# Performance work log

Measured on AMD Instinct MI355X. Metric: run time of the kernel, lower is better.

The kernel has to match this reference:

```python
import jax, jax.numpy as jnp
import numpy as np

SHRINK_THRES = 0.0025
EPS = 1e-12


def setup_inputs() -> dict:
    key = jax.random.key(0)
    k1, k2 = jax.random.split(key)
    N, C, H, W = 32, 256, 32, 32
    M = 2000
    x = jax.random.normal(k1, (N, C, H, W), dtype=jnp.float32)
    # torch init: uniform(-stdv, stdv), stdv = 1/sqrt(fea_dim)
    stdv = 1.0 / np.sqrt(C)
    weight = jax.random.uniform(k2, (M, C), dtype=jnp.float32, minval=-stdv, maxval=stdv)
    return {"x": x, "weight": weight}


def hard_shrink_relu(a, lambd=SHRINK_THRES, epsilon=EPS):
    d = a - lambd
    return jax.nn.relu(d) * a / (jnp.abs(d) + epsilon)


def reference(x, weight):
    N, C, H, W = x.shape
    M = weight.shape[0]
    # N x C x H x W -> (N*H*W) x C
    xt = jnp.transpose(x, (0, 2, 3, 1)).reshape(-1, C)  # (T, C)
    att = xt @ weight.T                                  # (T, M)
    att = jax.nn.softmax(att, axis=1)
    att = hard_shrink_relu(att)
    # L1 normalize over memory dim (torch F.normalize p=1, eps=1e-12)
    att = att / jnp.maximum(jnp.sum(jnp.abs(att), axis=1, keepdims=True), 1e-12)
    y = att @ weight                                     # (T, C)
    y = y.reshape(N, H, W, C).transpose(0, 3, 1, 2)      # N x C x H x W
    att = att.reshape(N, H, W, M).transpose(0, 3, 1, 2)  # N x M x H x W
    return (y, att)
```

## Files before the change

kernel.cpp:

```cpp
#include <hip/hip_runtime.h>

typedef _Float16 f16x8 __attribute__((ext_vector_type(8)));
typedef float    f32x4 __attribute__((ext_vector_type(4)));

constexpr int Nn = 32, Cc = 256, HW = 1024, Mm = 2000, Tt = 32768;
constexpr int TB = 64;
constexpr int XROW = 264;
constexpr int YROW = 257;
constexpr int LCAP = 768;
constexpr int NT = 63;
constexpr float LAMBDA = 0.0025f;
constexpr float PLO = LAMBDA * (1.0f - 3e-3f);
constexpr float PHI = LAMBDA * (1.0f + 3e-3f);
constexpr float ECUT = 4.8f;
constexpr float SCL = 4096.0f, ISCL = 1.0f / 4096.0f;

__global__ void wcvt_kernel(const float* __restrict__ w,
                            _Float16* __restrict__ whi, _Float16* __restrict__ wlo) {
  int i = blockIdx.x * 256 + threadIdx.x;
  if (i < Mm * Cc) {
    float v = w[i];
    _Float16 h = (_Float16)v;
    whi[i] = h;
    wlo[i] = (_Float16)((v - (float)h) * SCL);
  }
}

__device__ __forceinline__ void gl_lds16(const void* g, void* l) {
  __builtin_amdgcn_global_load_lds(
      (const __attribute__((address_space(1))) void*)g,
      (__attribute__((address_space(3))) void*)l, 16, 0, 0);
}

__global__ __launch_bounds__(512, 4)
void fused_mem_kernel(const float* __restrict__ x, const float* __restrict__ wgt,
                      const _Float16* __restrict__ whi, const _Float16* __restrict__ wlo,
                      float* __restrict__ y_out, float* __restrict__ att_out) {
  __shared__ __align__(16) float bufB[TB * XROW];
  __shared__ int   lm[LCAP];
  __shared__ float le[LCAP];
  __shared__ float la[LCAP];
  __shared__ float Zred[128];
  __shared__ float invZ[TB];
  __shared__ float l1s[TB];
  __shared__ float dens[TB];
  __shared__ int   lcnt;
  _Float16* Xh = (_Float16*)bufB;
  _Float16* Xl = Xh + TB * XROW;
  float*    yL = bufB;
  char*     Bb = (char*)bufB;

  const int tid = threadIdx.x;
  const int wv  = tid >> 6;
  const int l   = tid & 63;
  const int qw  = l >> 4;
  const int lr  = l & 15;
  const int tg  = wv & 3;
  const int mh  = wv >> 2;
  const int t0  = blockIdx.x * TB;
  const int n   = t0 >> 10;
  const int hw0 = t0 & 1023;

  if (tid == 0) lcnt = 0;
  if (tid < TB) l1s[tid] = 0.f;

  {
    const int h = tid & 63, cb = tid >> 6;
    const float* xp = x + ((size_t)n * Cc) * HW + hw0 + h;
    #pragma unroll
    for (int j = 0; j < 32; ++j) {
      int c = cb * 32 + j;
      float v = xp[(size_t)c * HW];
      _Float16 hh = (_Float16)v;
      Xh[h * XROW + c] = hh;
      Xl[h * XROW + c] = (_Float16)((v - (float)hh) * SCL);
    }
  }
  __syncthreads();

  f16x8 ahi[8], alo[8];
  #pragma unroll
  for (int ks = 0; ks < 8; ++ks) {
    ahi[ks] = *(const f16x8*)&Xh[(tg * 16 + lr) * XROW + ks * 32 + qw * 8];
    alo[ks] = *(const f16x8*)&Xl[(tg * 16 + lr) * XROW + ks * 32 + qw * 8];
  }
  __syncthreads();

  auto stage = [&](int b, int tile) {
    char* base = Bb + b * 32768;
    #pragma unroll
    for (int i = 0; i < 4; ++i) {
      const int bu = i * 512 + wv * 64;
      const int u2 = (bu + l) & 1023;
      const int row = u2 >> 5, chunk = u2 & 31;
      int mrow = tile * 32 + row; mrow = mrow < Mm ? mrow : (Mm - 1);
      const char* src = (const char*)(i < 2 ? whi : wlo)
                      + (size_t)mrow * 512 + ((chunk ^ (row & 7)) << 4);
      gl_lds16(src, base + bu * 16);
    }
  };

  stage(0, 0);
  __syncthreads();

  float zp[4] = {0.f, 0.f, 0.f, 0.f};
  const int rrow = mh * 16 + lr;
  const int rsw  = rrow & 7;
  int cur = 0;
  for (int t = 0; t < NT; ++t) {
    if (t + 1 < NT) stage(cur ^ 1, t + 1);

    {
      int m = t * 32 + (tid >> 4);
      if (m < Mm) {
        f32x4 z4 = {0.f, 0.f, 0.f, 0.f};
        *(f32x4*)(att_out + ((size_t)(n * Mm + m)) * HW + hw0 + ((tid & 15) << 2)) = z4;
      }
    }

    if (mh == 0 || t < NT - 1) {
      const char* bb = Bb + cur * 32768;
      f16x8 bh[8], bl[8];
      #pragma unroll
      for (int ks = 0; ks < 8; ++ks) {
        const int ch = (((ks * 4 + qw) ^ rsw) << 4);
        bh[ks] = *(const f16x8*)(bb + rrow * 512 + ch);
        bl[ks] = *(const f16x8*)(bb + 16384 + rrow * 512 + ch);
      }
      f32x4 ahh = {0.f, 0.f, 0.f, 0.f};
      f32x4 axl = {0.f, 0.f, 0.f, 0.f};
      f32x4 alh = {0.f, 0.f, 0.f, 0.f};
      #pragma unroll
      for (int ks = 0; ks < 8; ++ks) {
        ahh = __builtin_amdgcn_mfma_f32_16x16x32_f16(ahi[ks], bh[ks], ahh, 0, 0, 0);
        axl = __builtin_amdgcn_mfma_f32_16x16x32_f16(ahi[ks], bl[ks], axl, 0, 0, 0);
        alh = __builtin_amdgcn_mfma_f32_16x16x32_f16(alo[ks], bh[ks], alh, 0, 0, 0);
      }
      const int mrow_ = t * 32 + rrow;
      #pragma unroll
      for (int r = 0; r < 4; ++r) {
        float s = fmaf(axl[r] + alh[r], ISCL, ahh[r]);
        float e = __expf(s);
        zp[r] += e;
        if (e > ECUT) {
          int slot = atomicAdd(&lcnt, 1);
          if (slot < LCAP) { lm[slot] = ((tg * 16 + qw * 4 + r) << 16) | mrow_; le[slot] = e; }
        }
      }
    }
    __syncthreads();
    cur ^= 1;
  }

  #pragma unroll
  for (int o = 1; o < 16; o <<= 1)
    #pragma unroll
    for (int r = 0; r < 4; ++r) zp[r] += __shfl_xor(zp[r], o);
  if (lr == 0) {
    #pragma unroll
    for (int r = 0; r < 4; ++r) Zred[mh * 64 + tg * 16 + qw * 4 + r] = zp[r];
  }
  __syncthreads();

  if (tid < TB) invZ[tid] = 1.f / (Zred[tid] + Zred[64 + tid]);
  __syncthreads();

  const int ne = min(lcnt, LCAP);
  for (int e = tid; e < ne; e += 512) {
    const int tm = lm[e];
    const int t = tm >> 16, m = tm & 0xFFFF;
    float p = le[e] * invZ[t];
    float a = 0.f;
    if (p > PLO) {
      float pu = p;
      if (p < PHI) {
        const float* xr = x + ((size_t)n * Cc) * HW + hw0 + t;
        const float* wr = wgt + (size_t)m * Cc;
        float s = 0.f;
        for (int c = 0; c < Cc; ++c) s = fmaf(xr[(size_t)c * HW], wr[c], s);
        pu = expf(s) * invZ[t];
      }
      float d = pu - LAMBDA;
      if (d > 0.f) {
        a = (d * pu) / (d + 1e-12f);
        atomicAdd(&l1s[t], a);
      }
    }
    la[e] = a;
  }
  __syncthreads();

  if (tid < TB) dens[tid] = fmaxf(l1s[tid], 1e-12f);
  for (int i = tid; i < TB * YROW; i += 512) yL[i] = 0.f;
  __syncthreads();

  for (int e = wv; e < ne; e += 8) {
    float av = la[e];
    if (av > 0.f) {
      const int tm = lm[e];
      const int t = tm >> 16, m = tm & 0xFFFF;
      const float a = av / dens[t];
      float4 wf = *(const float4*)(wgt + (size_t)m * Cc + l * 4);
      float* yr = yL + t * YROW + l;
      atomicAdd(yr + 0,   a * wf.x);
      atomicAdd(yr + 64,  a * wf.y);
      atomicAdd(yr + 128, a * wf.z);
      atomicAdd(yr + 192, a * wf.w);
      if (l == 0)
        att_out[((size_t)(n * Mm + m)) * HW + hw0 + t] = a;
    }
  }
  __syncthreads();

  {
    const int h = tid & 63, cb = tid >> 6;
    float* yp = y_out + ((size_t)n * Cc) * HW + hw0 + h;
    #pragma unroll
    for (int j = 0; j < 32; ++j) {
      int c = cb * 32 + j;
      yp[(size_t)c * HW] = yL[h * YROW + (((c & 3) << 6) | (c >> 2))];
    }
  }
}

extern "C" void kernel_launch(void* const* d_in, const int* in_sizes, int n_in,
                              void* d_out, int out_size, void* d_ws, size_t ws_size,
                              hipStream_t stream) {
  const float* x = (const float*)d_in[0];
  const float* w = (const float*)d_in[1];
  float* y_out   = (float*)d_out;
  float* att_out = y_out + (size_t)Nn * Cc * HW;
  _Float16* whi = (_Float16*)d_ws;
  _Float16* wlo = whi + (size_t)Mm * Cc;

  wcvt_kernel<<<(Mm * Cc + 255) / 256, 256, 0, stream>>>(w, whi, wlo);
  fused_mem_kernel<<<Tt / TB, 512, 0, stream>>>(x, w, whi, wlo, y_out, att_out);
}
```

Before: 640.0 us.

## Widen memory tile to 64 rows with each wave computing two token subtiles

The weight tile streamed per iteration grows from 32 to 64 memory rows with double-buffered 64KB LDS stages, halving the iteration count and barriers. The warp layout is remapped so each wave covers 16 memory rows and two 16-token subtiles, reusing each loaded B fragment across two A fragments to cut LDS reads per MFMA. Softmax partial sums now reduce across four memory-row groups. In exchange, LDS use per block doubles and more A fragments stay live in registers, so occupancy drops (launch bounds lowered to 2 blocks per SM).

```diff
diff --git a/kernel.cpp b/kernel.cpp
--- a/kernel.cpp
+++ b/kernel.cpp
@@ -8,7 +8,7 @@
 constexpr int XROW = 264;
 constexpr int YROW = 257;
 constexpr int LCAP = 768;
-constexpr int NT = 63;
+constexpr int NT = 32;
 constexpr float LAMBDA = 0.0025f;
 constexpr float PLO = LAMBDA * (1.0f - 3e-3f);
 constexpr float PHI = LAMBDA * (1.0f + 3e-3f);
@@ -32,15 +32,15 @@
       (__attribute__((address_space(3))) void*)l, 16, 0, 0);
 }
 
-__global__ __launch_bounds__(512, 4)
+__global__ __launch_bounds__(512, 2)
 void fused_mem_kernel(const float* __restrict__ x, const float* __restrict__ wgt,
                       const _Float16* __restrict__ whi, const _Float16* __restrict__ wlo,
                       float* __restrict__ y_out, float* __restrict__ att_out) {
-  __shared__ __align__(16) float bufB[TB * XROW];
+  __shared__ __align__(16) float bufB[32768];
   __shared__ int   lm[LCAP];
   __shared__ float le[LCAP];
   __shared__ float la[LCAP];
-  __shared__ float Zred[128];
+  __shared__ float Zred[256];
   __shared__ float invZ[TB];
   __shared__ float l1s[TB];
   __shared__ float dens[TB];
@@ -55,8 +55,8 @@
   const int l   = tid & 63;
   const int qw  = l >> 4;
   const int lr  = l & 15;
-  const int tg  = wv & 3;
-  const int mh  = wv >> 2;
+  const int mh  = wv & 3;
+  const int tp  = wv >> 2;
   const int t0  = blockIdx.x * TB;
   const int n   = t0 >> 10;
   const int hw0 = t0 & 1023;
@@ -78,73 +78,94 @@
   }
   __syncthreads();
 
-  f16x8 ahi[8], alo[8];
+  f16x8 a0h[8], a0l[8], a1h[8], a1l[8];
   #pragma unroll
   for (int ks = 0; ks < 8; ++ks) {
-    ahi[ks] = *(const f16x8*)&Xh[(tg * 16 + lr) * XROW + ks * 32 + qw * 8];
-    alo[ks] = *(const f16x8*)&Xl[(tg * 16 + lr) * XROW + ks * 32 + qw * 8];
+    const int r0 = (tp * 32 + lr) * XROW + ks * 32 + qw * 8;
+    const int r1 = (tp * 32 + 16 + lr) * XROW + ks * 32 + qw * 8;
+    a0h[ks] = *(const f16x8*)&Xh[r0];
+    a0l[ks] = *(const f16x8*)&Xl[r0];
+    a1h[ks] = *(const f16x8*)&Xh[r1];
+    a1l[ks] = *(const f16x8*)&Xl[r1];
   }
   __syncthreads();
 
   auto stage = [&](int b, int tile) {
-    char* base = Bb + b * 32768;
-    #pragma unroll
-    for (int i = 0; i < 4; ++i) {
+    char* base = Bb + b * 65536;
+    #pragma unroll
+    for (int i = 0; i < 8; ++i) {
       const int bu = i * 512 + wv * 64;
-      const int u2 = (bu + l) & 1023;
-      const int row = u2 >> 5, chunk = u2 & 31;
-      int mrow = tile * 32 + row; mrow = mrow < Mm ? mrow : (Mm - 1);
-      const char* src = (const char*)(i < 2 ? whi : wlo)
-                      + (size_t)mrow * 512 + ((chunk ^ (row & 7)) << 4);
-      gl_lds16(src, base + bu * 16);
+      const int u2 = bu + l;
+      const int r64 = (u2 >> 5) & 63;
+      const int chunk = u2 & 31;
+      int mrow = tile * 64 + r64; mrow = mrow < Mm ? mrow : (Mm - 1);
+      const char* src = (const char*)(u2 < 2048 ? whi : wlo)
+                      + (size_t)mrow * 512 + ((chunk ^ (r64 & 7)) << 4);
+      gl_lds16(src, base + u2 * 16);
     }
   };
 
   stage(0, 0);
   __syncthreads();
 
-  float zp[4] = {0.f, 0.f, 0.f, 0.f};
+  float zp0[4] = {0.f, 0.f, 0.f, 0.f};
+  float zp1[4] = {0.f, 0.f, 0.f, 0.f};
   const int rrow = mh * 16 + lr;
   const int rsw  = rrow & 7;
   int cur = 0;
   for (int t = 0; t < NT; ++t) {
     if (t + 1 < NT) stage(cur ^ 1, t + 1);
 
-    {
-      int m = t * 32 + (tid >> 4);
+    #pragma unroll
+    for (int jj = 0; jj < 2; ++jj) {
+      int m = t * 64 + jj * 32 + (tid >> 4);
       if (m < Mm) {
         f32x4 z4 = {0.f, 0.f, 0.f, 0.f};
         *(f32x4*)(att_out + ((size_t)(n * Mm + m)) * HW + hw0 + ((tid & 15) << 2)) = z4;
       }
     }
 
-    if (mh == 0 || t < NT - 1) {
-      const char* bb = Bb + cur * 32768;
-      f16x8 bh[8], bl[8];
+    if (t < NT - 1 || mh == 0) {
+      const char* bb = Bb + cur * 65536;
+      f32x4 ahh0 = {0.f,0.f,0.f,0.f}, axl0 = {0.f,0.f,0.f,0.f}, alh0 = {0.f,0.f,0.f,0.f};
+      f32x4 ahh1 = {0.f,0.f,0.f,0.f}, axl1 = {0.f,0.f,0.f,0.f}, alh1 = {0.f,0.f,0.f,0.f};
       #pragma unroll
-      for (int ks = 0; ks < 8; ++ks) {
-        const int ch = (((ks * 4 + qw) ^ rsw) << 4);
-        bh[ks] = *(const f16x8*)(bb + rrow * 512 + ch);
-        bl[ks] = *(const f16x8*)(bb + 16384 + rrow * 512 + ch);
-      }
-      f32x4 ahh = {0.f, 0.f, 0.f, 0.f};
-      f32x4 axl = {0.f, 0.f, 0.f, 0.f};
-      f32x4 alh = {0.f, 0.f, 0.f, 0.f};
-      #pragma unroll
-      for (int ks = 0; ks < 8; ++ks) {
-        ahh = __builtin_amdgcn_mfma_f32_16x16x32_f16(ahi[ks], bh[ks], ahh, 0, 0, 0);
-        axl = __builtin_amdgcn_mfma_f32_16x16x32_f16(ahi[ks], bl[ks], axl, 0, 0, 0);
-        alh = __builtin_amdgcn_mfma_f32_16x16x32_f16(alo[ks], bh[ks], alh, 0, 0, 0);
-      }
-      const int mrow_ = t * 32 + rrow;
+      for (int kc = 0; kc < 2; ++kc) {
+        f16x8 bh[4], bl[4];
+        #pragma unroll
+        for (int k4 = 0; k4 < 4; ++k4) {
+          const int ks = kc * 4 + k4;
+          const int ch = rrow * 512 + (((ks * 4 + qw) ^ rsw) << 4);
+          bh[k4] = *(const f16x8*)(bb + ch);
+          bl[k4] = *(const f16x8*)(bb + 32768 + ch);
+        }
+        #pragma unroll
+        for (int k4 = 0; k4 < 4; ++k4) {
+          const int ks = kc * 4 + k4;
+          ahh0 = __builtin_amdgcn_mfma_f32_16x16x32_f16(a0h[ks], bh[k4], ahh0, 0, 0, 0);
+          axl0 = __builtin_amdgcn_mfma_f32_16x16x32_f16(a0h[ks], bl[k4], axl0, 0, 0, 0);
+          alh0 = __builtin_amdgcn_mfma_f32_16x16x32_f16(a0l[ks], bh[k4], alh0, 0, 0, 0);
+          ahh1 = __builtin_amdgcn_mfma_f32_16x16x32_f16(a1h[ks], bh[k4], ahh1, 0, 0, 0);
+          axl1 = __builtin_amdgcn_mfma_f32_16x16x32_f16(a1h[ks], bl[k4], axl1, 0, 0, 0);
+          alh1 = __builtin_amdgcn_mfma_f32_16x16x32_f16(a1l[ks], bh[k4], alh1, 0, 0, 0);
+        }
+      }
+      const int mrow_ = t * 64 + rrow;
       #pragma unroll
       for (int r = 0; r < 4; ++r) {
-        float s = fmaf(axl[r] + alh[r], ISCL, ahh[r]);
-        float e = __expf(s);
-        zp[r] += e;
-        if (e > ECUT) {
+        float s0 = fmaf(axl0[r] + alh0[r], ISCL, ahh0[r]);
+        float e0 = __expf(s0);
+        zp0[r] += e0;
+        if (e0 > ECUT) {
           int slot = atomicAdd(&lcnt, 1);
-          if (slot < LCAP) { lm[slot] = ((tg * 16 + qw * 4 + r) << 16) | mrow_; le[slot] = e; }
+          if (slot < LCAP) { lm[slot] = ((tp * 32 + qw * 4 + r) << 16) | mrow_; le[slot] = e0; }
+        }
+        float s1 = fmaf(axl1[r] + alh1[r], ISCL, ahh1[r]);
+        float e1 = __expf(s1);
+        zp1[r] += e1;
+        if (e1 > ECUT) {
+          int slot = atomicAdd(&lcnt, 1);
+          if (slot < LCAP) { lm[slot] = ((tp * 32 + 16 + qw * 4 + r) << 16) | mrow_; le[slot] = e1; }
         }
       }
     }
@@ -155,14 +176,21 @@
   #pragma unroll
   for (int o = 1; o < 16; o <<= 1)
     #pragma unroll
-    for (int r = 0; r < 4; ++r) zp[r] += __shfl_xor(zp[r], o);
+    for (int r = 0; r < 4; ++r) {
+      zp0[r] += __shfl_xor(zp0[r], o);
+      zp1[r] += __shfl_xor(zp1[r], o);
+    }
   if (lr == 0) {
     #pragma unroll
-    for (int r = 0; r < 4; ++r) Zred[mh * 64 + tg * 16 + qw * 4 + r] = zp[r];
-  }
-  __syncthreads();
-
-  if (tid < TB) invZ[tid] = 1.f / (Zred[tid] + Zred[64 + tid]);
+    for (int r = 0; r < 4; ++r) {
+      Zred[mh * 64 + tp * 32 + qw * 4 + r]      = zp0[r];
+      Zred[mh * 64 + tp * 32 + 16 + qw * 4 + r] = zp1[r];
+    }
+  }
+  __syncthreads();
+
+  if (tid < TB)
+    invZ[tid] = 1.f / (Zred[tid] + Zred[64 + tid] + Zred[128 + tid] + Zred[192 + tid]);
   __syncthreads();
 
   const int ne = min(lcnt, LCAP);
```

Result: faster. 588.4 us (-8.1%).
